# Optimization experiments

Measured on AMD Instinct MI355X. Metric: run time of the kernel, lower is better.

The kernel has to match this reference:

```python
import jax, jax.numpy as jnp
import numpy as np

SEQ = 4096
HIDDEN = 4096
HEAD_DIM = 1024
NUM_HEAD = HIDDEN // HEAD_DIM  # 4


def setup_inputs() -> dict:
    key = jax.random.key(0)
    ks = jax.random.split(key, 7)
    scale = 1.0 / np.sqrt(HIDDEN)  # torch Linear default-ish init scale
    h = jax.random.normal(ks[0], (SEQ, HIDDEN), dtype=jnp.float32)
    Wq = jax.random.normal(ks[1], (NUM_HEAD, HIDDEN, HEAD_DIM), dtype=jnp.float32) * scale
    bq = jax.random.normal(ks[2], (NUM_HEAD, HEAD_DIM), dtype=jnp.float32) * scale
    Wk = jax.random.normal(ks[3], (NUM_HEAD, HIDDEN, HEAD_DIM), dtype=jnp.float32) * scale
    bk = jax.random.normal(ks[4], (NUM_HEAD, HEAD_DIM), dtype=jnp.float32) * scale
    Wv = jax.random.normal(ks[5], (NUM_HEAD, HIDDEN, HEAD_DIM), dtype=jnp.float32) * scale
    bv = jax.random.normal(ks[6], (NUM_HEAD, HEAD_DIM), dtype=jnp.float32) * scale
    return {"h": h, "Wq": Wq, "bq": bq, "Wk": Wk, "bk": bk, "Wv": Wv, "bv": bv}


def reference(h, Wq, bq, Wk, bk, Wv, bv):
    # Batched per-head projections: q/k/v [H, S, E]
    q = jnp.einsum('sd,hde->hse', h, Wq) + bq[:, None, :]
    k = jnp.einsum('sd,hde->hse', h, Wk) + bk[:, None, :]
    v = jnp.einsum('sd,hde->hse', h, Wv) + bv[:, None, :]
    # Full (non-causal) attention scores [H, S, S], scaled by sqrt(head_dim)
    s = jnp.einsum('hse,hte->hst', q, k) / jnp.sqrt(jnp.asarray(HEAD_DIM, h.dtype))
    p = jax.nn.softmax(s, axis=-1)
    out = jnp.einsum('hst,hte->hse', p, v)  # [H, S, E]
    # Concatenate heads along feature dim -> [S, H*E]
    return jnp.transpose(out, (1, 0, 2)).reshape(h.shape[0], -1)
```

## Files before the change

### kernel.cpp

```cpp
#include <hip/hip_runtime.h>

#define SEQ   4096
#define HID   4096
#define EDIM  1024
#define NHEAD 4

typedef __attribute__((ext_vector_type(8))) short short8;
typedef __attribute__((ext_vector_type(16))) float f32x16;

typedef const __attribute__((address_space(1))) void* gas_ptr;
typedef __attribute__((address_space(3))) void* las_ptr;
#define GLD16(g, l) __builtin_amdgcn_global_load_lds((gas_ptr)(g), (las_ptr)(l), 16, 0, 0)

#define BARRIER() __builtin_amdgcn_s_barrier()
#define SCHED0()  __builtin_amdgcn_sched_barrier(0)
#define VMC0()    asm volatile("s_waitcnt vmcnt(0)" ::: "memory")

__device__ __forceinline__ unsigned short f2bf(float f) {
  union { float f; unsigned u; } v; v.f = f;
  unsigned r = v.u + 0x7fffu + ((v.u >> 16) & 1u);
  return (unsigned short)(r >> 16);
}
__device__ __forceinline__ float bf2f(unsigned short u) {
  union { unsigned u; float f; } v; v.u = ((unsigned)u) << 16;
  return v.f;
}

__global__ __launch_bounds__(256) void hconv_kernel(const float* __restrict__ in,
                                                    unsigned short* __restrict__ out) {
  size_t i = ((size_t)blockIdx.x * 256 + threadIdx.x) * 8;
  const float4 a = *(const float4*)(in + i);
  const float4 b = *(const float4*)(in + i + 4);
  short8 o;
  o[0] = (short)f2bf(a.x); o[1] = (short)f2bf(a.y);
  o[2] = (short)f2bf(a.z); o[3] = (short)f2bf(a.w);
  o[4] = (short)f2bf(b.x); o[5] = (short)f2bf(b.y);
  o[6] = (short)f2bf(b.z); o[7] = (short)f2bf(b.w);
  *(short8*)(out + i) = o;
}

__global__ __launch_bounds__(256) void wconv_kernel(const float* __restrict__ Wq,
                                                    const float* __restrict__ Wk,
                                                    const float* __restrict__ Wv,
                                                    unsigned short* __restrict__ wt) {
  const int mh = blockIdx.y;
  const int mat = mh >> 2, head = mh & 3;
  const float* W = (mat == 0 ? Wq : (mat == 1 ? Wk : Wv)) + (size_t)head * HID * EDIM;
  unsigned short* out = wt + (size_t)mh * EDIM * HID;
  const int tile = blockIdx.x;
  const int td = tile >> 4;
  const int te = tile & 15;
  __shared__ float lds[64][65];
  const int tid = threadIdx.x;
  const int r = tid >> 4, c4 = (tid & 15) * 4;
#pragma unroll
  for (int it = 0; it < 4; ++it) {
    int dr = r + 16 * it;
    const float4 v = *(const float4*)&W[(size_t)(td * 64 + dr) * EDIM + te * 64 + c4];
    lds[dr][c4 + 0] = v.x; lds[dr][c4 + 1] = v.y;
    lds[dr][c4 + 2] = v.z; lds[dr][c4 + 3] = v.w;
  }
  __syncthreads();
#pragma unroll
  for (int it = 0; it < 4; ++it) {
    int er = r + 16 * it;
    ushort4 o;
    o.x = f2bf(lds[c4 + 0][er]); o.y = f2bf(lds[c4 + 1][er]);
    o.z = f2bf(lds[c4 + 2][er]); o.w = f2bf(lds[c4 + 3][er]);
    *(ushort4*)&out[(size_t)(te * 64 + er) * HID + td * 64 + c4] = o;
  }
}

template <int MODE>
__global__ __launch_bounds__(512, 2) void gemm256_kernel(
    const unsigned short* __restrict__ Aall, const unsigned short* __restrict__ Ball,
    long long aBatch, long long bBatch, int K,
    const float* __restrict__ biasAll, long long biasBatch,
    void* __restrict__ outAll, long long outBatch, int ldOut, float scale,
    int gx, int gxy) {
  extern __shared__ char smem[];

  const int nwg = (int)gridDim.x;
  const int lin = (int)blockIdx.x;
  int wg = (lin & 7) * (nwg >> 3) + (lin >> 3);
  const int z = wg / gxy; wg -= z * gxy;
  const int by = wg / gx;
  const int bx = wg - by * gx;
  const int bm = by * 256, bn = bx * 256;

  const unsigned short* A = Aall + (size_t)z * aBatch;
  const unsigned short* B = Ball + (size_t)z * bBatch;

  const int tid = threadIdx.x;
  const int lane = tid & 63, wid = tid >> 6;
  const int wr = wid >> 2, wc = wid & 3;
  const int la31 = lane & 31, lg2 = lane >> 5;

  const int srow = tid >> 3;
  const int sk = ((tid & 7) ^ ((srow ^ (srow >> 3)) & 7)) * 8;
  const unsigned short* aS0 = A + (size_t)(bm +   0 + srow) * K + sk;
  const unsigned short* aS1 = A + (size_t)(bm +  64 + srow) * K + sk;
  const unsigned short* aS2 = A + (size_t)(bm + 128 + srow) * K + sk;
  const unsigned short* aS3 = A + (size_t)(bm + 192 + srow) * K + sk;
  const unsigned short* bS0 = B + (size_t)(bn +   0 + srow) * K + sk;
  const unsigned short* bS1 = B + (size_t)(bn +  64 + srow) * K + sk;
  const unsigned short* bS2 = B + (size_t)(bn + 128 + srow) * K + sk;
  const unsigned short* bS3 = B + (size_t)(bn + 192 + srow) * K + sk;

#define STG(tt)                                                           \
  do {                                                                    \
    char* _d = smem + (((tt) & 1) << 16) + tid * 16;                      \
    GLD16(aS0 + (size_t)(tt) * 64, _d);                                   \
    GLD16(aS1 + (size_t)(tt) * 64, _d + 8192);                            \
    GLD16(aS2 + (size_t)(tt) * 64, _d + 16384);                          \
    GLD16(aS3 + (size_t)(tt) * 64, _d + 24576);                          \
    GLD16(bS0 + (size_t)(tt) * 64, _d + 32768);                          \
    GLD16(bS1 + (size_t)(tt) * 64, _d + 40960);                          \
    GLD16(bS2 + (size_t)(tt) * 64, _d + 49152);                          \
    GLD16(bS3 + (size_t)(tt) * 64, _d + 57344);                          \
  } while (0)

  int aO[4], aX[4];
#pragma unroll
  for (int m = 0; m < 4; ++m) {
    const int arow = wr * 128 + m * 32 + la31;
    aO[m] = arow * 128;
    aX[m] = (arow ^ (arow >> 3)) & 7;
  }
  int bO[2], bX[2];
#pragma unroll
  for (int n = 0; n < 2; ++n) {
    const int brow = wc * 64 + n * 32 + la31;
    bO[n] = 32768 + brow * 128;
    bX[n] = (brow ^ (brow >> 3)) & 7;
  }

#define RD_A(SET, BASE, KS)                                               \
  _Pragma("unroll") for (int m = 0; m < 4; ++m)                           \
    SET[m] = *(const short8*)((BASE) + aO[m] +                            \
                              (((((KS) << 1) + lg2) ^ aX[m]) << 4));
#define RD_B(SET, BASE, KS)                                               \
  _Pragma("unroll") for (int n = 0; n < 2; ++n)                           \
    SET[n] = *(const short8*)((BASE) + bO[n] +                            \
                              (((((KS) << 1) + lg2) ^ bX[n]) << 4));
#define MFMA_S(AV, BV)                                                    \
  __builtin_amdgcn_s_setprio(1);                                          \
  _Pragma("unroll") for (int m = 0; m < 4; ++m)                           \
  _Pragma("unroll") for (int n = 0; n < 2; ++n)                           \
    acc[m][n] = __builtin_amdgcn_mfma_f32_32x32x16_bf16(                  \
        AV[m], BV[n], acc[m][n], 0, 0, 0);                                \
  __builtin_amdgcn_s_setprio(0);

  f32x16 acc[4][2];
#pragma unroll
  for (int m = 0; m < 4; ++m)
#pragma unroll
    for (int n = 0; n < 2; ++n)
#pragma unroll
      for (int r = 0; r < 16; ++r) acc[m][n][r] = 0.f;

  const int NT = K >> 6;

  short8 avA[4], bvA[2], avB[4], bvB[2];

  STG(0);
  VMC0();
  BARRIER();
  RD_A(avA, smem, 0); RD_B(bvA, smem, 0);
  SCHED0();

  for (int t = 0; t < NT; ++t) {
    const char* base  = smem + ((t & 1) << 16);
    const char* nbase = smem + (((t + 1) & 1) << 16);

    if (t + 1 < NT) STG(t + 1);
    RD_A(avB, base, 1); RD_B(bvB, base, 1);
    SCHED0();
    MFMA_S(avA, bvA);
    SCHED0();

    RD_A(avA, base, 2); RD_B(bvA, base, 2);
    SCHED0();
    MFMA_S(avB, bvB);
    SCHED0();

    RD_A(avB, base, 3); RD_B(bvB, base, 3);
    SCHED0();
    MFMA_S(avA, bvA);
    SCHED0();

    VMC0();
    BARRIER();
    if (t + 1 < NT) { RD_A(avA, nbase, 0); RD_B(bvA, nbase, 0); }
    SCHED0();
    MFMA_S(avB, bvB);
    SCHED0();
    BARRIER();
  }
#undef STG
#undef RD_A
#undef RD_B
#undef MFMA_S

  float bvv[2];
  if (MODE == 0 || MODE == 1) {
    const float* bias = biasAll + (size_t)z * biasBatch;
#pragma unroll
    for (int n = 0; n < 2; ++n) bvv[n] = bias[bn + wc * 64 + n * 32 + la31];
  }
#pragma unroll
  for (int m = 0; m < 4; ++m)
#pragma unroll
    for (int n = 0; n < 2; ++n)
#pragma unroll
      for (int r = 0; r < 16; ++r) {
        const int grow = bm + wr * 128 + m * 32 + (r & 3) + 8 * (r >> 2) + 4 * lg2;
        const int gcol = bn + wc * 64 + n * 32 + la31;
        float val = acc[m][n][r];
        if (MODE == 0 || MODE == 1) val += bvv[n];
        if (MODE == 2) val *= scale;
        if (MODE == 0 || MODE == 2) {
          unsigned short* o = (unsigned short*)outAll + (size_t)z * outBatch;
          o[(size_t)grow * ldOut + gcol] = f2bf(val);
        } else if (MODE == 1) {
          unsigned short* o = (unsigned short*)outAll + (size_t)z * outBatch;
          o[(size_t)gcol * ldOut + grow] = f2bf(val);
        } else {
          float* o = (float*)outAll + (size_t)z * outBatch;
          o[(size_t)grow * ldOut + gcol] = val;
        }
      }
}

__global__ __launch_bounds__(256) void softmax_kernel(unsigned short* __restrict__ Sb) {
  const size_t row = blockIdx.x;
  unsigned short* p = Sb + row * (size_t)SEQ;
  const int tid = threadIdx.x;
  const int lane = tid & 63, wid = tid >> 6;
  float v[16];
  const short8 u0 = *(const short8*)&p[tid * 16];
  const short8 u1 = *(const short8*)&p[tid * 16 + 8];
#pragma unroll
  for (int j = 0; j < 8; ++j) v[j] = bf2f((unsigned short)u0[j]);
#pragma unroll
  for (int j = 0; j < 8; ++j) v[8 + j] = bf2f((unsigned short)u1[j]);
  float mx = v[0];
#pragma unroll
  for (int j = 1; j < 16; ++j) mx = fmaxf(mx, v[j]);
#pragma unroll
  for (int off = 32; off; off >>= 1) mx = fmaxf(mx, __shfl_xor(mx, off));
  __shared__ float red[8];
  if (lane == 0) red[wid] = mx;
  __syncthreads();
  mx = fmaxf(fmaxf(red[0], red[1]), fmaxf(red[2], red[3]));
  float s = 0.f;
#pragma unroll
  for (int j = 0; j < 16; ++j) { v[j] = __expf(v[j] - mx); s += v[j]; }
#pragma unroll
  for (int off = 32; off; off >>= 1) s += __shfl_xor(s, off);
  if (lane == 0) red[4 + wid] = s;
  __syncthreads();
  s = (red[4] + red[5]) + (red[6] + red[7]);
  const float inv = 1.0f / s;
  short8 o0, o1;
#pragma unroll
  for (int j = 0; j < 8; ++j) o0[j] = (short)f2bf(v[j] * inv);
#pragma unroll
  for (int j = 0; j < 8; ++j) o1[j] = (short)f2bf(v[8 + j] * inv);
  *(short8*)&p[tid * 16] = o0;
  *(short8*)&p[tid * 16 + 8] = o1;
}

extern "C" void kernel_launch(void* const* d_in, const int* in_sizes, int n_in,
                              void* d_out, int out_size, void* d_ws, size_t ws_size,
                              hipStream_t stream) {
  const float* h  = (const float*)d_in[0];
  const float* Wq = (const float*)d_in[1];
  const float* bq = (const float*)d_in[2];
  const float* Wk = (const float*)d_in[3];
  const float* bk = (const float*)d_in[4];
  const float* Wv = (const float*)d_in[5];
  const float* bv = (const float*)d_in[6];
  float* out = (float*)d_out;
  char* ws = (char*)d_ws;

  (void)hipFuncSetAttribute((const void*)&gemm256_kernel<0>,
                            hipFuncAttributeMaxDynamicSharedMemorySize, 131072);
  (void)hipFuncSetAttribute((const void*)&gemm256_kernel<1>,
                            hipFuncAttributeMaxDynamicSharedMemorySize, 131072);
  (void)hipFuncSetAttribute((const void*)&gemm256_kernel<2>,
                            hipFuncAttributeMaxDynamicSharedMemorySize, 131072);
  (void)hipFuncSetAttribute((const void*)&gemm256_kernel<3>,
                            hipFuncAttributeMaxDynamicSharedMemorySize, 131072);

  unsigned short* hB = (unsigned short*)ws;
  unsigned short* wt = (unsigned short*)(ws + (32ull << 20));
  unsigned short* Sb = (unsigned short*)ws;
  unsigned short* Qb = (unsigned short*)(ws + (128ull << 20));
  unsigned short* Kb = (unsigned short*)(ws + (160ull << 20));
  unsigned short* Vt = (unsigned short*)(ws + (192ull << 20));

  const long long WED = (long long)EDIM * HID;
  const long long QKB = (long long)SEQ * EDIM;
  const long long SSB = (long long)SEQ * SEQ;

  hconv_kernel<<<dim3((SEQ * (size_t)HID) / (256 * 8)), 256, 0, stream>>>(h, hB);
  wconv_kernel<<<dim3((HID / 64) * (EDIM / 64), 12), 256, 0, stream>>>(Wq, Wk, Wv, wt);

  gemm256_kernel<0><<<dim3(4 * 16 * 4), 512, 131072, stream>>>(
      hB, wt + 0 * WED, 0, WED, HID, bq, EDIM, Qb, QKB, EDIM, 1.f, 4, 64);
  gemm256_kernel<0><<<dim3(4 * 16 * 4), 512, 131072, stream>>>(
      hB, wt + 4 * WED, 0, WED, HID, bk, EDIM, Kb, QKB, EDIM, 1.f, 4, 64);
  gemm256_kernel<1><<<dim3(4 * 16 * 4), 512, 131072, stream>>>(
      hB, wt + 8 * WED, 0, WED, HID, bv, EDIM, Vt, QKB, SEQ, 1.f, 4, 64);

  gemm256_kernel<2><<<dim3(16 * 16 * 4), 512, 131072, stream>>>(
      Qb, Kb, QKB, QKB, EDIM, nullptr, 0, Sb, SSB, SEQ, 0.03125f, 16, 256);

  softmax_kernel<<<dim3(NHEAD * SEQ), 256, 0, stream>>>(Sb);

  gemm256_kernel<3><<<dim3(4 * 16 * 4), 512, 131072, stream>>>(
      Sb, Vt, SSB, QKB, SEQ, nullptr, 0, out, (long long)EDIM, NHEAD * EDIM, 1.f, 4, 64);
}
```

Before: 783.3 us.

## Fuse QKV projections into one launch and fold softmax into GEMM epilogues

Merges the three Q/K/V projection GEMMs into a single batched launch that picks bias and output per z-slice, writing V transposed. When workspace allows, the score GEMM epilogue writes unnormalized exp(scaled scores) and atomically accumulates row sums. The PV GEMM divides by those sums, removing the separate softmax pass over the full score matrix. This skips max subtraction, so it relies on scores staying in a safe exponent range, and it adds atomics plus a memset.

```diff
diff --git a/kernel.cpp b/kernel.cpp
--- a/kernel.cpp
+++ b/kernel.cpp
@@ -75,9 +75,10 @@
 __global__ __launch_bounds__(512, 2) void gemm256_kernel(
     const unsigned short* __restrict__ Aall, const unsigned short* __restrict__ Ball,
     long long aBatch, long long bBatch, int K,
-    const float* __restrict__ biasAll, long long biasBatch,
-    void* __restrict__ outAll, long long outBatch, int ldOut, float scale,
-    int gx, int gxy) {
+    const float* __restrict__ b0, const float* __restrict__ b1,
+    const float* __restrict__ b2,
+    void* __restrict__ o0, void* __restrict__ o1, void* __restrict__ o2,
+    float* __restrict__ rowsum, float scale, int gx, int gxy) {
   extern __shared__ char smem[];
 
   const int nwg = (int)gridDim.x;
@@ -202,34 +203,58 @@
 #undef RD_B
 #undef MFMA_S
 
+  const long long QKB = (long long)SEQ * EDIM;
+  const long long SSB = (long long)SEQ * SEQ;
   float bvv[2];
-  if (MODE == 0 || MODE == 1) {
-    const float* bias = biasAll + (size_t)z * biasBatch;
+  if (MODE == 0) {
+    const int mat = z >> 2, head = z & 3;
+    const float* bias = (mat == 0 ? b0 : mat == 1 ? b1 : b2) + head * EDIM;
 #pragma unroll
     for (int n = 0; n < 2; ++n) bvv[n] = bias[bn + wc * 64 + n * 32 + la31];
   }
 #pragma unroll
   for (int m = 0; m < 4; ++m)
 #pragma unroll
-    for (int n = 0; n < 2; ++n)
-#pragma unroll
-      for (int r = 0; r < 16; ++r) {
-        const int grow = bm + wr * 128 + m * 32 + (r & 3) + 8 * (r >> 2) + 4 * lg2;
-        const int gcol = bn + wc * 64 + n * 32 + la31;
-        float val = acc[m][n][r];
-        if (MODE == 0 || MODE == 1) val += bvv[n];
-        if (MODE == 2) val *= scale;
-        if (MODE == 0 || MODE == 2) {
-          unsigned short* o = (unsigned short*)outAll + (size_t)z * outBatch;
-          o[(size_t)grow * ldOut + gcol] = f2bf(val);
-        } else if (MODE == 1) {
-          unsigned short* o = (unsigned short*)outAll + (size_t)z * outBatch;
-          o[(size_t)gcol * ldOut + grow] = f2bf(val);
+    for (int r = 0; r < 16; ++r) {
+      const int grow = bm + wr * 128 + m * 32 + (r & 3) + 8 * (r >> 2) + 4 * lg2;
+      const int col0 = bn + wc * 64 + la31;
+      float v0 = acc[m][0][r], v1 = acc[m][1][r];
+      if (MODE == 0) {
+        v0 += bvv[0]; v1 += bvv[1];
+        const int mat = z >> 2, head = z & 3;
+        if (mat == 2) {
+          unsigned short* o = (unsigned short*)o2 + (size_t)head * QKB;
+          o[(size_t)col0 * SEQ + grow]        = f2bf(v0);
+          o[(size_t)(col0 + 32) * SEQ + grow] = f2bf(v1);
         } else {
-          float* o = (float*)outAll + (size_t)z * outBatch;
-          o[(size_t)grow * ldOut + gcol] = val;
+          unsigned short* o =
+              (unsigned short*)(mat == 0 ? o0 : o1) + (size_t)head * QKB;
+          o[(size_t)grow * EDIM + col0]      = f2bf(v0);
+          o[(size_t)grow * EDIM + col0 + 32] = f2bf(v1);
         }
+      } else if (MODE == 2) {
+        unsigned short* o = (unsigned short*)o0 + (size_t)z * SSB;
+        if (rowsum) {
+          const float e0 = __expf(v0 * scale), e1 = __expf(v1 * scale);
+          o[(size_t)grow * SEQ + col0]      = f2bf(e0);
+          o[(size_t)grow * SEQ + col0 + 32] = f2bf(e1);
+          float rp = e0 + e1;
+          rp += __shfl_xor(rp, 1);  rp += __shfl_xor(rp, 2);
+          rp += __shfl_xor(rp, 4);  rp += __shfl_xor(rp, 8);
+          rp += __shfl_xor(rp, 16);
+          if (la31 == 0) atomicAdd(&rowsum[(size_t)z * SEQ + grow], rp);
+        } else {
+          o[(size_t)grow * SEQ + col0]      = f2bf(v0 * scale);
+          o[(size_t)grow * SEQ + col0 + 32] = f2bf(v1 * scale);
+        }
+      } else {
+        float rinv = 1.0f;
+        if (rowsum) rinv = 1.0f / rowsum[(size_t)z * SEQ + grow];
+        float* o = (float*)o0 + (size_t)z * EDIM;
+        o[(size_t)grow * (NHEAD * EDIM) + col0]      = v0 * rinv;
+        o[(size_t)grow * (NHEAD * EDIM) + col0 + 32] = v1 * rinv;
       }
+    }
 }
 
 __global__ __launch_bounds__(256) void softmax_kernel(unsigned short* __restrict__ Sb) {
@@ -286,8 +311,6 @@
 
   (void)hipFuncSetAttribute((const void*)&gemm256_kernel<0>,
                             hipFuncAttributeMaxDynamicSharedMemorySize, 131072);
-  (void)hipFuncSetAttribute((const void*)&gemm256_kernel<1>,
-                            hipFuncAttributeMaxDynamicSharedMemorySize, 131072);
   (void)hipFuncSetAttribute((const void*)&gemm256_kernel<2>,
                             hipFuncAttributeMaxDynamicSharedMemorySize, 131072);
   (void)hipFuncSetAttribute((const void*)&gemm256_kernel<3>,
@@ -299,6 +322,8 @@
   unsigned short* Qb = (unsigned short*)(ws + (128ull << 20));
   unsigned short* Kb = (unsigned short*)(ws + (160ull << 20));
   unsigned short* Vt = (unsigned short*)(ws + (192ull << 20));
+  float* rowsum = (float*)(ws + (224ull << 20));
+  const bool fused = ws_size >= (224ull << 20) + (size_t)NHEAD * SEQ * sizeof(float);
 
   const long long WED = (long long)EDIM * HID;
   const long long QKB = (long long)SEQ * EDIM;
@@ -306,19 +331,20 @@
 
   hconv_kernel<<<dim3((SEQ * (size_t)HID) / (256 * 8)), 256, 0, stream>>>(h, hB);
   wconv_kernel<<<dim3((HID / 64) * (EDIM / 64), 12), 256, 0, stream>>>(Wq, Wk, Wv, wt);
-
-  gemm256_kernel<0><<<dim3(4 * 16 * 4), 512, 131072, stream>>>(
-      hB, wt + 0 * WED, 0, WED, HID, bq, EDIM, Qb, QKB, EDIM, 1.f, 4, 64);
-  gemm256_kernel<0><<<dim3(4 * 16 * 4), 512, 131072, stream>>>(
-      hB, wt + 4 * WED, 0, WED, HID, bk, EDIM, Kb, QKB, EDIM, 1.f, 4, 64);
-  gemm256_kernel<1><<<dim3(4 * 16 * 4), 512, 131072, stream>>>(
-      hB, wt + 8 * WED, 0, WED, HID, bv, EDIM, Vt, QKB, SEQ, 1.f, 4, 64);
-
-  gemm256_kernel<2><<<dim3(16 * 16 * 4), 512, 131072, stream>>>(
-      Qb, Kb, QKB, QKB, EDIM, nullptr, 0, Sb, SSB, SEQ, 0.03125f, 16, 256);
-
-  softmax_kernel<<<dim3(NHEAD * SEQ), 256, 0, stream>>>(Sb);
-
-  gemm256_kernel<3><<<dim3(4 * 16 * 4), 512, 131072, stream>>>(
-      Sb, Vt, SSB, QKB, SEQ, nullptr, 0, out, (long long)EDIM, NHEAD * EDIM, 1.f, 4, 64);
-}
+  if (fused)
+    hipMemsetAsync(rowsum, 0, (size_t)NHEAD * SEQ * sizeof(float), stream);
+
+  gemm256_kernel<0><<<dim3(768), 512, 131072, stream>>>(
+      hB, wt, 0, WED, HID, bq, bk, bv, Qb, Kb, Vt, nullptr, 1.f, 4, 64);
+
+  gemm256_kernel<2><<<dim3(1024), 512, 131072, stream>>>(
+      Qb, Kb, QKB, QKB, EDIM, nullptr, nullptr, nullptr, Sb, nullptr, nullptr,
+      fused ? rowsum : nullptr, 0.03125f, 16, 256);
+
+  if (!fused)
+    softmax_kernel<<<dim3(NHEAD * SEQ), 256, 0, stream>>>(Sb);
+
+  gemm256_kernel<3><<<dim3(256), 512, 131072, stream>>>(
+      Sb, Vt, SSB, QKB, SEQ, nullptr, nullptr, nullptr, out, nullptr, nullptr,
+      fused ? rowsum : nullptr, 1.f, 4, 64);
+}
```

Measured after the change: 989.4 us. 1.26x slower.

## Run GEMM with 1024 threads per block and smaller per-wave tiles

Applied to the files above, without the earlier changes.

The GEMM kernel moves from 512 to 1024 threads per 256x256 tile, so each of 16 waves computes a 64x64 sub-tile with half the accumulators. The staging load count per thread halves. The software-pipelined register double-buffering of LDS reads is replaced by a simpler loop: wait, barrier, prefetch the next stage, then read and compute in two halves with lgkmcnt waits. This trades intra-wave latency hiding for more waves, and it raises the LDS read volume because each B fragment is now read by more waves.

```diff
diff --git a/kernel.cpp b/kernel.cpp
--- a/kernel.cpp
+++ b/kernel.cpp
@@ -14,6 +14,7 @@
 
 #define BARRIER() __builtin_amdgcn_s_barrier()
 #define SCHED0()  __builtin_amdgcn_sched_barrier(0)
+#define LGKM0()   asm volatile("s_waitcnt lgkmcnt(0)" ::: "memory")
 #define VMC0()    asm volatile("s_waitcnt vmcnt(0)" ::: "memory")
 
 __device__ __forceinline__ unsigned short f2bf(float f) {
@@ -72,7 +73,7 @@
 }
 
 template <int MODE>
-__global__ __launch_bounds__(512, 2) void gemm256_kernel(
+__global__ __launch_bounds__(1024, 4) void gemm1024_kernel(
     const unsigned short* __restrict__ Aall, const unsigned short* __restrict__ Ball,
     long long aBatch, long long bBatch, int K,
     const float* __restrict__ biasAll, long long biasBatch,
@@ -98,32 +99,24 @@
 
   const int srow = tid >> 3;
   const int sk = ((tid & 7) ^ ((srow ^ (srow >> 3)) & 7)) * 8;
-  const unsigned short* aS0 = A + (size_t)(bm +   0 + srow) * K + sk;
-  const unsigned short* aS1 = A + (size_t)(bm +  64 + srow) * K + sk;
-  const unsigned short* aS2 = A + (size_t)(bm + 128 + srow) * K + sk;
-  const unsigned short* aS3 = A + (size_t)(bm + 192 + srow) * K + sk;
-  const unsigned short* bS0 = B + (size_t)(bn +   0 + srow) * K + sk;
-  const unsigned short* bS1 = B + (size_t)(bn +  64 + srow) * K + sk;
-  const unsigned short* bS2 = B + (size_t)(bn + 128 + srow) * K + sk;
-  const unsigned short* bS3 = B + (size_t)(bn + 192 + srow) * K + sk;
+  const unsigned short* aS0 = A + (size_t)(bm + srow) * K + sk;
+  const unsigned short* aS1 = aS0 + (size_t)128 * K;
+  const unsigned short* bS0 = B + (size_t)(bn + srow) * K + sk;
+  const unsigned short* bS1 = bS0 + (size_t)128 * K;
 
 #define STG(tt)                                                           \
   do {                                                                    \
     char* _d = smem + (((tt) & 1) << 16) + tid * 16;                      \
     GLD16(aS0 + (size_t)(tt) * 64, _d);                                   \
-    GLD16(aS1 + (size_t)(tt) * 64, _d + 8192);                            \
-    GLD16(aS2 + (size_t)(tt) * 64, _d + 16384);                          \
-    GLD16(aS3 + (size_t)(tt) * 64, _d + 24576);                          \
+    GLD16(aS1 + (size_t)(tt) * 64, _d + 16384);                          \
     GLD16(bS0 + (size_t)(tt) * 64, _d + 32768);                          \
-    GLD16(bS1 + (size_t)(tt) * 64, _d + 40960);                          \
-    GLD16(bS2 + (size_t)(tt) * 64, _d + 49152);                          \
-    GLD16(bS3 + (size_t)(tt) * 64, _d + 57344);                          \
+    GLD16(bS1 + (size_t)(tt) * 64, _d + 49152);                          \
   } while (0)
 
-  int aO[4], aX[4];
-#pragma unroll
-  for (int m = 0; m < 4; ++m) {
-    const int arow = wr * 128 + m * 32 + la31;
+  int aO[2], aX[2];
+#pragma unroll
+  for (int m = 0; m < 2; ++m) {
+    const int arow = wr * 64 + m * 32 + la31;
     aO[m] = arow * 128;
     aX[m] = (arow ^ (arow >> 3)) & 7;
   }
@@ -135,25 +128,31 @@
     bX[n] = (brow ^ (brow >> 3)) & 7;
   }
 
-#define RD_A(SET, BASE, KS)                                               \
-  _Pragma("unroll") for (int m = 0; m < 4; ++m)                           \
-    SET[m] = *(const short8*)((BASE) + aO[m] +                            \
-                              (((((KS) << 1) + lg2) ^ aX[m]) << 4));
-#define RD_B(SET, BASE, KS)                                               \
-  _Pragma("unroll") for (int n = 0; n < 2; ++n)                           \
-    SET[n] = *(const short8*)((BASE) + bO[n] +                            \
-                              (((((KS) << 1) + lg2) ^ bX[n]) << 4));
-#define MFMA_S(AV, BV)                                                    \
+#define RD2(S0, S1)                                                       \
+  _Pragma("unroll") for (int m = 0; m < 2; ++m) {                         \
+    av[m][0] = *(const short8*)(base + aO[m] +                            \
+                                (((((S0) << 1) + lg2) ^ aX[m]) << 4));    \
+    av[m][1] = *(const short8*)(base + aO[m] +                            \
+                                (((((S1) << 1) + lg2) ^ aX[m]) << 4));    \
+  }                                                                       \
+  _Pragma("unroll") for (int n = 0; n < 2; ++n) {                         \
+    bv[n][0] = *(const short8*)(base + bO[n] +                            \
+                                (((((S0) << 1) + lg2) ^ bX[n]) << 4));    \
+    bv[n][1] = *(const short8*)(base + bO[n] +                            \
+                                (((((S1) << 1) + lg2) ^ bX[n]) << 4));    \
+  }
+#define MFMA8()                                                           \
   __builtin_amdgcn_s_setprio(1);                                          \
-  _Pragma("unroll") for (int m = 0; m < 4; ++m)                           \
+  _Pragma("unroll") for (int s = 0; s < 2; ++s)                           \
+  _Pragma("unroll") for (int m = 0; m < 2; ++m)                           \
   _Pragma("unroll") for (int n = 0; n < 2; ++n)                           \
     acc[m][n] = __builtin_amdgcn_mfma_f32_32x32x16_bf16(                  \
-        AV[m], BV[n], acc[m][n], 0, 0, 0);                                \
+        av[m][s], bv[n][s], acc[m][n], 0, 0, 0);                          \
   __builtin_amdgcn_s_setprio(0);
 
-  f32x16 acc[4][2];
-#pragma unroll
-  for (int m = 0; m < 4; ++m)
+  f32x16 acc[2][2];
+#pragma unroll
+  for (int m = 0; m < 2; ++m)
 #pragma unroll
     for (int n = 0; n < 2; ++n)
 #pragma unroll
@@ -161,46 +160,32 @@
 
   const int NT = K >> 6;
 
-  short8 avA[4], bvA[2], avB[4], bvB[2];
+  short8 av[2][2], bv[2][2];
 
   STG(0);
-  VMC0();
-  BARRIER();
-  RD_A(avA, smem, 0); RD_B(bvA, smem, 0);
-  SCHED0();
 
   for (int t = 0; t < NT; ++t) {
-    const char* base  = smem + ((t & 1) << 16);
-    const char* nbase = smem + (((t + 1) & 1) << 16);
-
-    if (t + 1 < NT) STG(t + 1);
-    RD_A(avB, base, 1); RD_B(bvB, base, 1);
-    SCHED0();
-    MFMA_S(avA, bvA);
-    SCHED0();
-
-    RD_A(avA, base, 2); RD_B(bvA, base, 2);
-    SCHED0();
-    MFMA_S(avB, bvB);
-    SCHED0();
-
-    RD_A(avB, base, 3); RD_B(bvB, base, 3);
-    SCHED0();
-    MFMA_S(avA, bvA);
-    SCHED0();
+    const char* base = smem + ((t & 1) << 16);
 
     VMC0();
     BARRIER();
-    if (t + 1 < NT) { RD_A(avA, nbase, 0); RD_B(bvA, nbase, 0); }
+    if (t + 1 < NT) STG(t + 1);
+
+    RD2(0, 1);
+    LGKM0();
     SCHED0();
-    MFMA_S(avB, bvB);
+    MFMA8();
     SCHED0();
-    BARRIER();
+
+    RD2(2, 3);
+    LGKM0();
+    SCHED0();
+    MFMA8();
+    SCHED0();
   }
 #undef STG
-#undef RD_A
-#undef RD_B
-#undef MFMA_S
+#undef RD2
+#undef MFMA8
 
   float bvv[2];
   if (MODE == 0 || MODE == 1) {
@@ -209,12 +194,12 @@
     for (int n = 0; n < 2; ++n) bvv[n] = bias[bn + wc * 64 + n * 32 + la31];
   }
 #pragma unroll
-  for (int m = 0; m < 4; ++m)
+  for (int m = 0; m < 2; ++m)
 #pragma unroll
     for (int n = 0; n < 2; ++n)
 #pragma unroll
       for (int r = 0; r < 16; ++r) {
-        const int grow = bm + wr * 128 + m * 32 + (r & 3) + 8 * (r >> 2) + 4 * lg2;
+        const int grow = bm + wr * 64 + m * 32 + (r & 3) + 8 * (r >> 2) + 4 * lg2;
         const int gcol = bn + wc * 64 + n * 32 + la31;
         float val = acc[m][n][r];
         if (MODE == 0 || MODE == 1) val += bvv[n];
@@ -284,13 +269,13 @@
   float* out = (float*)d_out;
   char* ws = (char*)d_ws;
 
-  (void)hipFuncSetAttribute((const void*)&gemm256_kernel<0>,
+  (void)hipFuncSetAttribute((const void*)&gemm1024_kernel<0>,
                             hipFuncAttributeMaxDynamicSharedMemorySize, 131072);
-  (void)hipFuncSetAttribute((const void*)&gemm256_kernel<1>,
+  (void)hipFuncSetAttribute((const void*)&gemm1024_kernel<1>,
                             hipFuncAttributeMaxDynamicSharedMemorySize, 131072);
-  (void)hipFuncSetAttribute((const void*)&gemm256_kernel<2>,
+  (void)hipFuncSetAttribute((const void*)&gemm1024_kernel<2>,
                             hipFuncAttributeMaxDynamicSharedMemorySize, 131072);
-  (void)hipFuncSetAttribute((const void*)&gemm256_kernel<3>,
+  (void)hipFuncSetAttribute((const void*)&gemm1024_kernel<3>,
                             hipFuncAttributeMaxDynamicSharedMemorySize, 131072);
 
   unsigned short* hB = (unsigned short*)ws;
@@ -307,18 +292,18 @@
   hconv_kernel<<<dim3((SEQ * (size_t)HID) / (256 * 8)), 256, 0, stream>>>(h, hB);
   wconv_kernel<<<dim3((HID / 64) * (EDIM / 64), 12), 256, 0, stream>>>(Wq, Wk, Wv, wt);
 
-  gemm256_kernel<0><<<dim3(4 * 16 * 4), 512, 131072, stream>>>(
+  gemm1024_kernel<0><<<dim3(4 * 16 * 4), 1024, 131072, stream>>>(
       hB, wt + 0 * WED, 0, WED, HID, bq, EDIM, Qb, QKB, EDIM, 1.f, 4, 64);
-  gemm256_kernel<0><<<dim3(4 * 16 * 4), 512, 131072, stream>>>(
+  gemm1024_kernel<0><<<dim3(4 * 16 * 4), 1024, 131072, stream>>>(
       hB, wt + 4 * WED, 0, WED, HID, bk, EDIM, Kb, QKB, EDIM, 1.f, 4, 64);
-  gemm256_kernel<1><<<dim3(4 * 16 * 4), 512, 131072, stream>>>(
+  gemm1024_kernel<1><<<dim3(4 * 16 * 4), 1024, 131072, stream>>>(
       hB, wt + 8 * WED, 0, WED, HID, bv, EDIM, Vt, QKB, SEQ, 1.f, 4, 64);
 
-  gemm256_kernel<2><<<dim3(16 * 16 * 4), 512, 131072, stream>>>(
+  gemm1024_kernel<2><<<dim3(16 * 16 * 4), 1024, 131072, stream>>>(
       Qb, Kb, QKB, QKB, EDIM, nullptr, 0, Sb, SSB, SEQ, 0.03125f, 16, 256);
 
   softmax_kernel<<<dim3(NHEAD * SEQ), 256, 0, stream>>>(Sb);
 
-  gemm256_kernel<3><<<dim3(4 * 16 * 4), 512, 131072, stream>>>(
+  gemm1024_kernel<3><<<dim3(4 * 16 * 4), 1024, 131072, stream>>>(
       Sb, Vt, SSB, QKB, SEQ, nullptr, 0, out, (long long)EDIM, NHEAD * EDIM, 1.f, 4, 64);
 }
```

Result: slower. 898.4 us (+14.7%).
